# Optimization experiments

Hardware: AMD Instinct MI355X
Metric: run time of the kernel (lower is better)

## Reference

```python
import jax, jax.numpy as jnp
import numpy as np

D_MODEL = 1024
NUM_HEADS = 16
HEAD_DIM = D_MODEL // NUM_HEADS


def setup_inputs() -> dict:
    key = jax.random.key(0)
    k1, k2, k3, k4, k5 = jax.random.split(key, 5)
    scale = 1.0 / np.sqrt(D_MODEL)
    x = jax.random.normal(k1, (2, 2048, D_MODEL), dtype=jnp.float32)
    Wqkv = jax.random.uniform(k2, (D_MODEL, 3 * D_MODEL), jnp.float32, -scale, scale)
    bqkv = jax.random.uniform(k3, (3 * D_MODEL,), jnp.float32, -scale, scale)
    Wout = jax.random.uniform(k4, (D_MODEL, D_MODEL), jnp.float32, -scale, scale)
    bout = jax.random.uniform(k5, (D_MODEL,), jnp.float32, -scale, scale)
    return {"x": x, "Wqkv": Wqkv, "bqkv": bqkv, "Wout": Wout, "bout": bout}


def reference(x, Wqkv, bqkv, Wout, bout):
    B, S, _ = x.shape
    qkv = x @ Wqkv + bqkv                                   # [B, S, 3*D]
    # reshape to [B, S, H, 3*head_dim] then to [B, H, S, 3*head_dim]
    qkv = qkv.reshape(B, S, NUM_HEADS, 3 * HEAD_DIM).transpose(0, 2, 1, 3)
    q, k, v = jnp.split(qkv, 3, axis=-1)                    # each [B, H, S, hd]
    scaled = jnp.einsum("bhqd,bhkd->bhqk", q, k) / jnp.sqrt(jnp.float32(HEAD_DIM))
    attn = jax.nn.softmax(scaled, axis=-1)                  # [B, H, S, S]
    values = jnp.einsum("bhqk,bhkd->bhqd", attn, v)         # [B, H, S, hd]
    values = values.transpose(0, 2, 1, 3).reshape(B, S, D_MODEL)
    return values @ Wout + bout
```

## Files before the change

### kernel.cpp

```cpp
#include <hip/hip_runtime.h>


typedef __attribute__((ext_vector_type(8)))  short short8;
typedef __attribute__((ext_vector_type(4)))  short short4v;
typedef __attribute__((ext_vector_type(8)))  float float8;
typedef __attribute__((ext_vector_type(4)))  float f32x4;
typedef __attribute__((ext_vector_type(16))) float f32x16;
typedef __attribute__((ext_vector_type(4)))  int   int4v;

#define D_MODEL 1024
#define NHEAD   16
#define HD      64
#define SEQ     2048
#define N3      (3*D_MODEL)
#define MB      (1024*1024)

static __device__ __forceinline__ float bf2f(short s) {
    unsigned u = ((unsigned)(unsigned short)s) << 16;
    return __builtin_bit_cast(float, u);
}
static __device__ __forceinline__ short f2bf(float f) {
    unsigned u = __builtin_bit_cast(unsigned, f);
    u = (u + 0x7fff + ((u >> 16) & 1)) >> 16;
    return (short)u;
}
static __device__ __forceinline__ unsigned cvtpk(float a, float b) {
    unsigned r;
    asm("v_cvt_pk_bf16_f32 %0, %1, %2" : "=v"(r) : "v"(a), "v"(b));
    return r;
}
static __device__ __forceinline__ void gl16(const short* g, short* l) {
    __builtin_amdgcn_global_load_lds(
        (const __attribute__((address_space(1))) unsigned int*)g,
        (__attribute__((address_space(3))) unsigned int*)l, 16, 0, 0);
}

__global__ __launch_bounds__(256) void prep(
    const float* __restrict__ x, const float* __restrict__ Wqkv,
    const float* __restrict__ Wout,
    short* __restrict__ Xh, short* __restrict__ Xl,
    short* __restrict__ Wh, short* __restrict__ Wl,
    short* __restrict__ Woh, short* __restrict__ Wol)
{
    __shared__ float tile[32][33];
    const int bid = blockIdx.x;
    const int tid = threadIdx.x;

    if (bid < 2048) {
        const int i = (bid * 256 + tid) * 8;
        const float8 v = *(const float8*)&x[i];
        short8 h, l;
#pragma unroll
        for (int j = 0; j < 8; ++j) {
            h[j] = f2bf(v[j]);
            l[j] = f2bf(v[j] - bf2f(h[j]));
        }
        *(short8*)&Xh[i] = h;
        *(short8*)&Xl[i] = l;
        return;
    }

    const float* in; short *hi, *lo; int K, N, bx, by;
    if (bid < 5120) {
        const int b2 = bid - 2048;
        in = Wqkv; hi = Wh; lo = Wl; K = D_MODEL; N = N3;
        bx = b2 % 96; by = b2 / 96;
    } else {
        const int b3 = bid - 5120;
        in = Wout; hi = Woh; lo = Wol; K = D_MODEL; N = D_MODEL;
        bx = b3 & 31; by = b3 >> 5;
    }
    const int n0 = bx * 32, k0 = by * 32;
    const int tx = tid & 31, ty = tid >> 5;
#pragma unroll
    for (int i = 0; i < 4; ++i)
        tile[ty + 8*i][tx] = in[(k0 + ty + 8*i) * N + (n0 + tx)];
    __syncthreads();
#pragma unroll
    for (int i = 0; i < 4; ++i) {
        const float v  = tile[tx][ty + 8*i];
        const short vh = f2bf(v);
        const short vl = f2bf(v - bf2f(vh));
        const int idx  = (n0 + ty + 8*i) * K + (k0 + tx);
        hi[idx] = vh;
        lo[idx] = vl;
    }
}

#define QBUF_SH 20480
#define OFF_AL  4096
#define OFF_BH  8192
#define OFF_BL  14336

__global__ __launch_bounds__(512, 4) void qkv_gemm8(
    const short* __restrict__ Xh, const short* __restrict__ Xl,
    const short* __restrict__ Bh, const short* __restrict__ Bl,
    const float* __restrict__ bias,
    short* __restrict__ Qo, short* __restrict__ Ko, short* __restrict__ Vt)
{
    __shared__ __attribute__((aligned(16))) short smem[2 * QBUF_SH];

    const int tid  = threadIdx.x;
    const int wave = tid >> 6, lane = tid & 63;
    const int q4 = lane >> 4, l16 = lane & 15;
    const int wr = wave >> 2, wc = wave & 3;
    const int csw = (q4 ^ ((l16 ^ (l16 >> 2)) & 3)) * 8;

    const int flat = blockIdx.x;
    const int sw = (flat & 7) * 64 + (flat >> 3);
    const int mt = sw & 31, nt = sw >> 5;
    const int m0 = mt * 128, n0 = nt * 192;

    const short* srcp[5];
#pragma unroll
    for (int j = 0; j < 5; ++j) {
        const int id = j * 512 + tid;
        int r; const short* mat; int row0;
        if (id < 512)       { r = id >> 2;          mat = Xh; row0 = m0; }
        else if (id < 1024) { r = (id - 512) >> 2;  mat = Xl; row0 = m0; }
        else if (id < 1792) { r = (id - 1024) >> 2; mat = Bh; row0 = n0; }
        else                { r = (id - 1792) >> 2; mat = Bl; row0 = n0; }
        const int cg = (id & 3) ^ ((r ^ (r >> 2)) & 3);
        srcp[j] = &mat[(size_t)(row0 + r) * D_MODEL + cg * 8];
    }

    auto stage = [&](int b) {
#pragma unroll
        for (int j = 0; j < 5; ++j) {
            gl16(srcp[j], smem + b * QBUF_SH + (j * 512 + tid) * 8);
            srcp[j] += 32;
        }
    };

    f32x4 acc[4][3];
#pragma unroll
    for (int i = 0; i < 4; ++i)
#pragma unroll
        for (int j = 0; j < 3; ++j) acc[i][j] = (f32x4){0.f, 0.f, 0.f, 0.f};

    stage(0);
    asm volatile("s_waitcnt vmcnt(0)" ::: "memory");
    __builtin_amdgcn_s_barrier();

    for (int t = 0; t < 32; ++t) {
        const int cur = t & 1;
        const short* base = smem + cur * QBUF_SH;
        const short* Ah_s = base;
        const short* Al_s = base + OFF_AL;
        const short* Bh_s = base + OFF_BH;
        const short* Bl_s = base + OFF_BL;

        short8 bhf[3], blf[3], a0h[2], a0l[2];
#pragma unroll
        for (int n = 0; n < 3; ++n) {
            const int rb = (wc * 48 + n * 16 + l16) * 32 + csw;
            bhf[n] = *(const short8*)(Bh_s + rb);
            blf[n] = *(const short8*)(Bl_s + rb);
        }
#pragma unroll
        for (int ti = 0; ti < 2; ++ti) {
            const int ra = (wr * 64 + ti * 16 + l16) * 32 + csw;
            a0h[ti] = *(const short8*)(Ah_s + ra);
            a0l[ti] = *(const short8*)(Al_s + ra);
        }
        if (t < 31) stage(cur ^ 1);
        __builtin_amdgcn_s_barrier();
        asm volatile("s_waitcnt lgkmcnt(0)" ::: "memory");
        __builtin_amdgcn_sched_barrier(0);
        short8 a1h[2], a1l[2];
#pragma unroll
        for (int ti = 0; ti < 2; ++ti) {
            const int ra = (wr * 64 + (2 + ti) * 16 + l16) * 32 + csw;
            a1h[ti] = *(const short8*)(Ah_s + ra);
            a1l[ti] = *(const short8*)(Al_s + ra);
        }
        __builtin_amdgcn_sched_barrier(0);
        __builtin_amdgcn_s_setprio(1);
#pragma unroll
        for (int ti = 0; ti < 2; ++ti)
#pragma unroll
            for (int n = 0; n < 3; ++n) {
                acc[ti][n] = __builtin_amdgcn_mfma_f32_16x16x32_bf16(a0h[ti], bhf[n], acc[ti][n], 0, 0, 0);
                acc[ti][n] = __builtin_amdgcn_mfma_f32_16x16x32_bf16(a0h[ti], blf[n], acc[ti][n], 0, 0, 0);
                acc[ti][n] = __builtin_amdgcn_mfma_f32_16x16x32_bf16(a0l[ti], bhf[n], acc[ti][n], 0, 0, 0);
            }
        __builtin_amdgcn_s_setprio(0);
        __builtin_amdgcn_s_barrier();

        asm volatile("s_waitcnt lgkmcnt(0)" ::: "memory");
        __builtin_amdgcn_sched_barrier(0);
        __builtin_amdgcn_s_setprio(1);
#pragma unroll
        for (int ti = 0; ti < 2; ++ti)
#pragma unroll
            for (int n = 0; n < 3; ++n) {
                acc[2+ti][n] = __builtin_amdgcn_mfma_f32_16x16x32_bf16(a1h[ti], bhf[n], acc[2+ti][n], 0, 0, 0);
                acc[2+ti][n] = __builtin_amdgcn_mfma_f32_16x16x32_bf16(a1h[ti], blf[n], acc[2+ti][n], 0, 0, 0);
                acc[2+ti][n] = __builtin_amdgcn_mfma_f32_16x16x32_bf16(a1l[ti], bhf[n], acc[2+ti][n], 0, 0, 0);
            }
        __builtin_amdgcn_s_setprio(0);
        asm volatile("s_waitcnt vmcnt(0)" ::: "memory");
        __builtin_amdgcn_s_barrier();
    }

    const float SCALE_Q = 0.125f * 1.4426950408889634f;
#pragma unroll
    for (int tj = 0; tj < 3; ++tj) {
        const int jj = wc * 48 + tj * 16 + l16;
        const int n  = nt * 192 + jj;
        const float bv = bias[n];
#pragma unroll
        for (int ti = 0; ti < 4; ++ti) {
            const int mb = m0 + wr * 64 + ti * 16 + q4 * 4;
            const int b = mb >> 11;
            const int s = mb & 2047;
            const int bh_ = b * NHEAD + nt;
            if (jj >= 128) {
                short4v v4;
#pragma unroll
                for (int r = 0; r < 4; ++r) v4[r] = f2bf(acc[ti][tj][r] + bv);
                *(short4v*)&Vt[(bh_ * HD + (jj - 128)) * SEQ + s] = v4;
            } else if (jj < 64) {
#pragma unroll
                for (int r = 0; r < 4; ++r)
                    Qo[(bh_ * SEQ + s + r) * HD + jj] = f2bf((acc[ti][tj][r] + bv) * SCALE_Q);
            } else {
#pragma unroll
                for (int r = 0; r < 4; ++r)
                    Ko[(bh_ * SEQ + s + r) * HD + (jj - 64)] = f2bf(acc[ti][tj][r] + bv);
            }
        }
    }
}

__global__ __launch_bounds__(256, 2) void attn_tscore(
    const short* __restrict__ Q, const short* __restrict__ K,
    const short* __restrict__ Vt,
    short* __restrict__ Ch, short* __restrict__ Cl)
{
    __shared__ __attribute__((aligned(16))) char smem[36864];
    short (*Ks)[72] = (short(*)[72])smem;
    short (*Vs)[72] = (short(*)[72])(smem + 18432);

    const int bh = blockIdx.x;
    const int qb = blockIdx.y;
    const int bi = bh >> 4, hi_ = bh & 15;

    const short* Qp  = Q  + bh * SEQ * HD;
    const short* Kp  = K  + bh * SEQ * HD;
    const short* Vtp = Vt + bh * HD * SEQ;

    const int tid  = threadIdx.x;
    const int wave = tid >> 6, lane = tid & 63;
    const int l5 = lane & 31, hf = lane >> 5;
    const int q0w = qb * 128 + wave * 32;

    short8 qf[4];
#pragma unroll
    for (int c = 0; c < 4; ++c)
        qf[c] = *(const short8*)&Qp[(q0w + l5) * HD + c * 16 + hf * 8];

    f32x16 oacc0 = (f32x16)(0.f), oacc1 = (f32x16)(0.f);
    float m = -1.0e30f, l = 0.f;

    const int sr = tid >> 2;
    const int sc = (tid & 3) * 16;

    short8 kr0 = *(const short8*)&Kp[sr * HD + sc];
    short8 kr1 = *(const short8*)&Kp[sr * HD + sc + 8];
    short8 vr0 = *(const short8*)&Vtp[sr * SEQ + sc];
    short8 vr1 = *(const short8*)&Vtp[sr * SEQ + sc + 8];
    *(short8*)&Ks[sr][sc]     = kr0;
    *(short8*)&Ks[sr][sc + 8] = kr1;
    *(short8*)&Vs[sr][sc]     = vr0;
    *(short8*)&Vs[sr][sc + 8] = vr1;
    __syncthreads();

    for (int kc = 0; kc < 32; ++kc) {
        const int buf = (kc & 1) << 6;

        if (kc < 31) {
            const int nkb = (kc + 1) << 6;
            kr0 = *(const short8*)&Kp[(nkb + sr) * HD + sc];
            kr1 = *(const short8*)&Kp[(nkb + sr) * HD + sc + 8];
            vr0 = *(const short8*)&Vtp[sr * SEQ + nkb + sc];
            vr1 = *(const short8*)&Vtp[sr * SEQ + nkb + sc + 8];
        }

        f32x16 s0 = (f32x16)(0.f), s1 = (f32x16)(0.f);
#pragma unroll
        for (int c = 0; c < 4; ++c) {
            const short8 ka0 = *(const short8*)&Ks[buf + l5][c * 16 + hf * 8];
            const short8 ka1 = *(const short8*)&Ks[buf + 32 + l5][c * 16 + hf * 8];
            s0 = __builtin_amdgcn_mfma_f32_32x32x16_bf16(ka0, qf[c], s0, 0, 0, 0);
            s1 = __builtin_amdgcn_mfma_f32_32x32x16_bf16(ka1, qf[c], s1, 0, 0, 0);
        }

        float t[8];
#pragma unroll
        for (int i = 0; i < 8; ++i)
            t[i] = fmaxf(fmaxf(s0[i], s0[i + 8]), fmaxf(s1[i], s1[i + 8]));
        float pmax = fmaxf(fmaxf(fmaxf(t[0], t[1]), fmaxf(t[2], t[3])),
                           fmaxf(fmaxf(t[4], t[5]), fmaxf(t[6], t[7])));
        pmax = fmaxf(pmax, __shfl_xor(pmax, 32, 64));

        if (!__all(pmax - m <= 8.0f)) {
            const float mnew  = fmaxf(m, pmax);
            const float alpha = exp2f(m - mnew);
#pragma unroll
            for (int i = 0; i < 16; ++i) { oacc0[i] *= alpha; oacc1[i] *= alpha; }
            l *= alpha;
            m = mnew;
        }

        float p0[16], p1[16];
#pragma unroll
        for (int i = 0; i < 16; ++i) { p0[i] = exp2f(s0[i] - m); p1[i] = exp2f(s1[i] - m); }
        float sa = 0.f, sb = 0.f, sc_ = 0.f, sd = 0.f;
#pragma unroll
        for (int i = 0; i < 4; ++i) {
            sa += p0[i] + p0[i + 8];
            sb += p0[i + 4] + p0[i + 12];
            sc_ += p1[i] + p1[i + 8];
            sd += p1[i + 4] + p1[i + 12];
        }
        float rs = (sa + sb) + (sc_ + sd);
        rs += __shfl_xor(rs, 32, 64);
        l += rs;

        unsigned u0 = cvtpk(p0[0],  p0[1]),  u1 = cvtpk(p0[2],  p0[3]);
        unsigned u2 = cvtpk(p0[4],  p0[5]),  u3 = cvtpk(p0[6],  p0[7]);
        unsigned u4 = cvtpk(p0[8],  p0[9]),  u5 = cvtpk(p0[10], p0[11]);
        unsigned u6 = cvtpk(p0[12], p0[13]), u7 = cvtpk(p0[14], p0[15]);
        unsigned w0 = cvtpk(p1[0],  p1[1]),  w1 = cvtpk(p1[2],  p1[3]);
        unsigned w2 = cvtpk(p1[4],  p1[5]),  w3 = cvtpk(p1[6],  p1[7]);
        unsigned w4 = cvtpk(p1[8],  p1[9]),  w5 = cvtpk(p1[10], p1[11]);
        unsigned w6 = cvtpk(p1[12], p1[13]), w7 = cvtpk(p1[14], p1[15]);
        const unsigned x0 = __shfl_xor(u0, 32, 64), x1 = __shfl_xor(u1, 32, 64);
        const unsigned x2 = __shfl_xor(u2, 32, 64), x3 = __shfl_xor(u3, 32, 64);
        const unsigned x4 = __shfl_xor(u4, 32, 64), x5 = __shfl_xor(u5, 32, 64);
        const unsigned x6 = __shfl_xor(u6, 32, 64), x7 = __shfl_xor(u7, 32, 64);
        const unsigned y0 = __shfl_xor(w0, 32, 64), y1 = __shfl_xor(w1, 32, 64);
        const unsigned y2 = __shfl_xor(w2, 32, 64), y3 = __shfl_xor(w3, 32, 64);
        const unsigned y4 = __shfl_xor(w4, 32, 64), y5 = __shfl_xor(w5, 32, 64);
        const unsigned y6 = __shfl_xor(w6, 32, 64), y7 = __shfl_xor(w7, 32, 64);
        int4v pb0 = (int4v){ (int)(hf ? x2 : u0), (int)(hf ? x3 : u1),
                             (int)(hf ? u2 : x0), (int)(hf ? u3 : x1) };
        int4v pb1 = (int4v){ (int)(hf ? x6 : u4), (int)(hf ? x7 : u5),
                             (int)(hf ? u6 : x4), (int)(hf ? u7 : x5) };
        int4v pb2 = (int4v){ (int)(hf ? y2 : w0), (int)(hf ? y3 : w1),
                             (int)(hf ? w2 : y0), (int)(hf ? w3 : y1) };
        int4v pb3 = (int4v){ (int)(hf ? y6 : w4), (int)(hf ? y7 : w5),
                             (int)(hf ? w6 : y4), (int)(hf ? w7 : y5) };
        const short8 pbf0 = __builtin_bit_cast(short8, pb0);
        const short8 pbf1 = __builtin_bit_cast(short8, pb1);
        const short8 pbf2 = __builtin_bit_cast(short8, pb2);
        const short8 pbf3 = __builtin_bit_cast(short8, pb3);

        {
            const short8 va0 = *(const short8*)&Vs[buf + l5][hf * 8];
            const short8 va1 = *(const short8*)&Vs[buf + l5][16 + hf * 8];
            const short8 va2 = *(const short8*)&Vs[buf + l5][32 + hf * 8];
            const short8 va3 = *(const short8*)&Vs[buf + l5][48 + hf * 8];
            oacc0 = __builtin_amdgcn_mfma_f32_32x32x16_bf16(va0, pbf0, oacc0, 0, 0, 0);
            oacc0 = __builtin_amdgcn_mfma_f32_32x32x16_bf16(va1, pbf1, oacc0, 0, 0, 0);
            oacc0 = __builtin_amdgcn_mfma_f32_32x32x16_bf16(va2, pbf2, oacc0, 0, 0, 0);
            oacc0 = __builtin_amdgcn_mfma_f32_32x32x16_bf16(va3, pbf3, oacc0, 0, 0, 0);
            const short8 vb0 = *(const short8*)&Vs[buf + 32 + l5][hf * 8];
            const short8 vb1 = *(const short8*)&Vs[buf + 32 + l5][16 + hf * 8];
            const short8 vb2 = *(const short8*)&Vs[buf + 32 + l5][32 + hf * 8];
            const short8 vb3 = *(const short8*)&Vs[buf + 32 + l5][48 + hf * 8];
            oacc1 = __builtin_amdgcn_mfma_f32_32x32x16_bf16(vb0, pbf0, oacc1, 0, 0, 0);
            oacc1 = __builtin_amdgcn_mfma_f32_32x32x16_bf16(vb1, pbf1, oacc1, 0, 0, 0);
            oacc1 = __builtin_amdgcn_mfma_f32_32x32x16_bf16(vb2, pbf2, oacc1, 0, 0, 0);
            oacc1 = __builtin_amdgcn_mfma_f32_32x32x16_bf16(vb3, pbf3, oacc1, 0, 0, 0);
        }

        if (kc < 31) {
            const int wb = ((kc + 1) & 1) << 6;
            *(short8*)&Ks[wb + sr][sc]     = kr0;
            *(short8*)&Ks[wb + sr][sc + 8] = kr1;
            *(short8*)&Vs[wb + sr][sc]     = vr0;
            *(short8*)&Vs[wb + sr][sc + 8] = vr1;
        }
        __syncthreads();
    }

    const float inv = 1.0f / l;
#pragma unroll
    for (int i = 0; i < 16; ++i) { oacc0[i] *= inv; oacc1[i] *= inv; }

    float (*epi)[68] = (float(*)[68])(smem + wave * 8704);
#pragma unroll
    for (int r = 0; r < 16; ++r) {
        const int d = (r & 3) + 8 * (r >> 2) + 4 * hf;
        epi[l5][d]      = oacc0[r];
        epi[l5][32 + d] = oacc1[r];
    }
    __builtin_amdgcn_s_waitcnt(0);
#pragma unroll
    for (int pass = 0; pass < 8; ++pass) {
        const int row = pass * 4 + (lane >> 4);
        const int col = (lane & 15) * 4;
        const float4 v = *(const float4*)&epi[row][col];
        const float o[4] = {v.x, v.y, v.z, v.w};
        short4v hh, ll;
#pragma unroll
        for (int i = 0; i < 4; ++i) {
            hh[i] = f2bf(o[i]);
            ll[i] = f2bf(o[i] - bf2f(hh[i]));
        }
        const size_t co = ((size_t)(bi * SEQ + q0w + row)) * D_MODEL + hi_ * HD + col;
        *(short4v*)&Ch[co] = hh;
        *(short4v*)&Cl[co] = ll;
    }
}

__global__ __launch_bounds__(256) void out_gemm128(
    const short* __restrict__ Ah, const short* __restrict__ Al,
    const short* __restrict__ Bh, const short* __restrict__ Bl,
    const float* __restrict__ bias, float* __restrict__ out)
{
    __shared__ short AhS[128*32], AlS[128*32], BhS[128*32], BlS[128*32];

    const int tid  = threadIdx.x;
    const int wave = tid >> 6, lane = tid & 63;
    const int q4 = lane >> 4, l16 = lane & 15;
    const int m0 = blockIdx.y * 128, n0 = blockIdx.x * 128;
    const int rw = (wave & 1) * 64, cw = (wave >> 1) * 64;
    const int trow = tid >> 2;
    const int tcol = (((tid & 3) ^ ((trow ^ (trow >> 2)) & 3))) * 8;
    const int csw = (q4 ^ ((l16 ^ (l16 >> 2)) & 3)) * 8;

    f32x4 acc[4][4];
#pragma unroll
    for (int i = 0; i < 4; ++i)
#pragma unroll
        for (int j = 0; j < 4; ++j) acc[i][j] = (f32x4){0.f, 0.f, 0.f, 0.f};

    for (int kt = 0; kt < D_MODEL; kt += 32) {
        gl16(&Ah[(m0 + trow) * D_MODEL + kt + tcol],      AhS + tid * 8);
        gl16(&Ah[(m0 + 64 + trow) * D_MODEL + kt + tcol], AhS + 2048 + tid * 8);
        gl16(&Al[(m0 + trow) * D_MODEL + kt + tcol],      AlS + tid * 8);
        gl16(&Al[(m0 + 64 + trow) * D_MODEL + kt + tcol], AlS + 2048 + tid * 8);
        gl16(&Bh[(n0 + trow) * D_MODEL + kt + tcol],      BhS + tid * 8);
        gl16(&Bh[(n0 + 64 + trow) * D_MODEL + kt + tcol], BhS + 2048 + tid * 8);
        gl16(&Bl[(n0 + trow) * D_MODEL + kt + tcol],      BlS + tid * 8);
        gl16(&Bl[(n0 + 64 + trow) * D_MODEL + kt + tcol], BlS + 2048 + tid * 8);
        __syncthreads();

        short8 ah[4], al[4], bh[4], bl[4];
#pragma unroll
        for (int t = 0; t < 4; ++t) {
            const int ra = (rw + t * 16 + l16) * 32 + csw;
            const int rb = (cw + t * 16 + l16) * 32 + csw;
            ah[t] = *(const short8*)&AhS[ra];
            al[t] = *(const short8*)&AlS[ra];
            bh[t] = *(const short8*)&BhS[rb];
            bl[t] = *(const short8*)&BlS[rb];
        }
#pragma unroll
        for (int ti = 0; ti < 4; ++ti)
#pragma unroll
            for (int tj = 0; tj < 4; ++tj) {
                acc[ti][tj] = __builtin_amdgcn_mfma_f32_16x16x32_bf16(ah[ti], bh[tj], acc[ti][tj], 0, 0, 0);
                acc[ti][tj] = __builtin_amdgcn_mfma_f32_16x16x32_bf16(ah[ti], bl[tj], acc[ti][tj], 0, 0, 0);
                acc[ti][tj] = __builtin_amdgcn_mfma_f32_16x16x32_bf16(al[ti], bh[tj], acc[ti][tj], 0, 0, 0);
            }
        __syncthreads();
    }

#pragma unroll
    for (int tj = 0; tj < 4; ++tj) {
        const int n = n0 + cw + tj * 16 + l16;
        const float bv = bias[n];
#pragma unroll
        for (int ti = 0; ti < 4; ++ti) {
            const int mb = m0 + rw + ti * 16 + q4 * 4;
#pragma unroll
            for (int r = 0; r < 4; ++r)
                out[(mb + r) * D_MODEL + n] = acc[ti][tj][r] + bv;
        }
    }
}

extern "C" void kernel_launch(void* const* d_in, const int* in_sizes, int n_in,
                              void* d_out, int out_size, void* d_ws, size_t ws_size,
                              hipStream_t stream)
{
    const float* x    = (const float*)d_in[0];
    const float* Wqkv = (const float*)d_in[1];
    const float* bqkv = (const float*)d_in[2];
    const float* Wout = (const float*)d_in[3];
    const float* bout = (const float*)d_in[4];
    float* out = (float*)d_out;

    char* ws = (char*)d_ws;
    short* Qb  = (short*)(ws);
    short* Kb  = (short*)(ws +  8*MB);
    short* Vtb = (short*)(ws + 16*MB);
    short* Woh = (short*)(ws + 24*MB);
    short* Wol = (short*)(ws + 26*MB);
    short* Ch  = (short*)(ws + 28*MB);
    short* Cl  = (short*)(ws + 36*MB);
    short* Xh  = (short*)(ws + 44*MB);
    short* Xl  = (short*)(ws + 52*MB);
    short* Wh  = (short*)(ws + 60*MB);
    short* Wl  = (short*)(ws + 66*MB);

    prep<<<6144, 256, 0, stream>>>(x, Wqkv, Wout, Xh, Xl, Wh, Wl, Woh, Wol);
    qkv_gemm8<<<dim3(512), 512, 0, stream>>>(Xh, Xl, Wh, Wl, bqkv, Qb, Kb, Vtb);
    attn_tscore<<<dim3(32, 16), 256, 0, stream>>>(Qb, Kb, Vtb, Ch, Cl);
    out_gemm128<<<dim3(8, 32), 256, 0, stream>>>(Ch, Cl, Woh, Wol, bout, out);
}
```

Measured before the change: 285.6 us.

## Split attention over two KV halves with merge kernel; use permlane32 swap

The attention kernel now splits the key/value sequence into two halves along a new grid dimension. That doubles the block count from 512 to 1024, to fill the GPU better. Each half writes unnormalized fp32 partial outputs plus running max and sum. A new merge kernel then rescales, combines and emits the bf16 hi/lo split. The 16 cross-half shuffles plus selects are replaced with v_permlane32_swap instructions. The cost is an extra kernel launch, fp32 partial traffic, and workspace aliasing whose buffer reuse ordering must hold.

```diff
diff --git a/kernel.cpp b/kernel.cpp
--- a/kernel.cpp
+++ b/kernel.cpp
@@ -29,6 +29,8 @@
     asm("v_cvt_pk_bf16_f32 %0, %1, %2" : "=v"(r) : "v"(a), "v"(b));
     return r;
 }
+#define PLSWAP(a, b) asm("v_permlane32_swap_b32 %0, %1" : "+v"(a), "+v"(b))
+
 static __device__ __forceinline__ void gl16(const short* g, short* l) {
     __builtin_amdgcn_global_load_lds(
         (const __attribute__((address_space(1))) unsigned int*)g,
@@ -236,19 +238,19 @@
 __global__ __launch_bounds__(256, 2) void attn_tscore(
     const short* __restrict__ Q, const short* __restrict__ K,
     const short* __restrict__ Vt,
-    short* __restrict__ Ch, short* __restrict__ Cl)
+    float* __restrict__ Opart, float2* __restrict__ Ml)
 {
     __shared__ __attribute__((aligned(16))) char smem[36864];
     short (*Ks)[72] = (short(*)[72])smem;
     short (*Vs)[72] = (short(*)[72])(smem + 18432);
 
-    const int bh = blockIdx.x;
-    const int qb = blockIdx.y;
-    const int bi = bh >> 4, hi_ = bh & 15;
-
-    const short* Qp  = Q  + bh * SEQ * HD;
-    const short* Kp  = K  + bh * SEQ * HD;
-    const short* Vtp = Vt + bh * HD * SEQ;
+    const int bh  = blockIdx.x;
+    const int qb  = blockIdx.y;
+    const int kvz = blockIdx.z;
+
+    const short* Qp  = Q  + (size_t)bh * SEQ * HD;
+    const short* Kp  = K  + (size_t)bh * SEQ * HD + (size_t)kvz * 1024 * HD;
+    const short* Vtp = Vt + (size_t)bh * HD * SEQ + (size_t)kvz * 1024;
 
     const int tid  = threadIdx.x;
     const int wave = tid >> 6, lane = tid & 63;
@@ -276,10 +278,10 @@
     *(short8*)&Vs[sr][sc + 8] = vr1;
     __syncthreads();
 
-    for (int kc = 0; kc < 32; ++kc) {
+    for (int kc = 0; kc < 16; ++kc) {
         const int buf = (kc & 1) << 6;
 
-        if (kc < 31) {
+        if (kc < 15) {
             const int nkb = (kc + 1) << 6;
             kr0 = *(const short8*)&Kp[(nkb + sr) * HD + sc];
             kr1 = *(const short8*)&Kp[(nkb + sr) * HD + sc + 8];
@@ -336,22 +338,12 @@
         unsigned w2 = cvtpk(p1[4],  p1[5]),  w3 = cvtpk(p1[6],  p1[7]);
         unsigned w4 = cvtpk(p1[8],  p1[9]),  w5 = cvtpk(p1[10], p1[11]);
         unsigned w6 = cvtpk(p1[12], p1[13]), w7 = cvtpk(p1[14], p1[15]);
-        const unsigned x0 = __shfl_xor(u0, 32, 64), x1 = __shfl_xor(u1, 32, 64);
-        const unsigned x2 = __shfl_xor(u2, 32, 64), x3 = __shfl_xor(u3, 32, 64);
-        const unsigned x4 = __shfl_xor(u4, 32, 64), x5 = __shfl_xor(u5, 32, 64);
-        const unsigned x6 = __shfl_xor(u6, 32, 64), x7 = __shfl_xor(u7, 32, 64);
-        const unsigned y0 = __shfl_xor(w0, 32, 64), y1 = __shfl_xor(w1, 32, 64);
-        const unsigned y2 = __shfl_xor(w2, 32, 64), y3 = __shfl_xor(w3, 32, 64);
-        const unsigned y4 = __shfl_xor(w4, 32, 64), y5 = __shfl_xor(w5, 32, 64);
-        const unsigned y6 = __shfl_xor(w6, 32, 64), y7 = __shfl_xor(w7, 32, 64);
-        int4v pb0 = (int4v){ (int)(hf ? x2 : u0), (int)(hf ? x3 : u1),
-                             (int)(hf ? u2 : x0), (int)(hf ? u3 : x1) };
-        int4v pb1 = (int4v){ (int)(hf ? x6 : u4), (int)(hf ? x7 : u5),
-                             (int)(hf ? u6 : x4), (int)(hf ? u7 : x5) };
-        int4v pb2 = (int4v){ (int)(hf ? y2 : w0), (int)(hf ? y3 : w1),
-                             (int)(hf ? w2 : y0), (int)(hf ? w3 : y1) };
-        int4v pb3 = (int4v){ (int)(hf ? y6 : w4), (int)(hf ? y7 : w5),
-                             (int)(hf ? w6 : y4), (int)(hf ? w7 : y5) };
+        PLSWAP(u0, u2); PLSWAP(u1, u3); PLSWAP(u4, u6); PLSWAP(u5, u7);
+        PLSWAP(w0, w2); PLSWAP(w1, w3); PLSWAP(w4, w6); PLSWAP(w5, w7);
+        int4v pb0 = (int4v){ (int)u0, (int)u1, (int)u2, (int)u3 };
+        int4v pb1 = (int4v){ (int)u4, (int)u5, (int)u6, (int)u7 };
+        int4v pb2 = (int4v){ (int)w0, (int)w1, (int)w2, (int)w3 };
+        int4v pb3 = (int4v){ (int)w4, (int)w5, (int)w6, (int)w7 };
         const short8 pbf0 = __builtin_bit_cast(short8, pb0);
         const short8 pbf1 = __builtin_bit_cast(short8, pb1);
         const short8 pbf2 = __builtin_bit_cast(short8, pb2);
@@ -376,7 +368,7 @@
             oacc1 = __builtin_amdgcn_mfma_f32_32x32x16_bf16(vb3, pbf3, oacc1, 0, 0, 0);
         }
 
-        if (kc < 31) {
+        if (kc < 15) {
             const int wb = ((kc + 1) & 1) << 6;
             *(short8*)&Ks[wb + sr][sc]     = kr0;
             *(short8*)&Ks[wb + sr][sc + 8] = kr1;
@@ -386,29 +378,76 @@
         __syncthreads();
     }
 
-    const float inv = 1.0f / l;
-#pragma unroll
-    for (int i = 0; i < 16; ++i) { oacc0[i] *= inv; oacc1[i] *= inv; }
-
-    float (*epi)[68] = (float(*)[68])(smem + wave * 8704);
+    float* Op = Opart + ((((size_t)kvz * 32 + bh) * 16 + qb) * 4 + wave) * 2048;
+#pragma unroll
+    for (int r = 0; r < 4; ++r) {
+        float4 v;
+        v.x = oacc0[4*r]; v.y = oacc0[4*r+1]; v.z = oacc0[4*r+2]; v.w = oacc0[4*r+3];
+        *(float4*)&Op[r * 256 + lane * 4] = v;
+    }
+#pragma unroll
+    for (int r = 0; r < 4; ++r) {
+        float4 v;
+        v.x = oacc1[4*r]; v.y = oacc1[4*r+1]; v.z = oacc1[4*r+2]; v.w = oacc1[4*r+3];
+        *(float4*)&Op[(4 + r) * 256 + lane * 4] = v;
+    }
+    if (hf == 0) {
+        float2 mv; mv.x = m; mv.y = l;
+        Ml[((size_t)kvz * 32 + bh) * 2048 + q0w + l5] = mv;
+    }
+}
+
+__global__ __launch_bounds__(256) void attn_merge(
+    const float* __restrict__ Opart, const float2* __restrict__ Ml,
+    short* __restrict__ Ch, short* __restrict__ Cl)
+{
+    __shared__ float epi[4][32][68];
+    const int tid = threadIdx.x, wave = tid >> 6, lane = tid & 63;
+    const int l5 = lane & 31, hf = lane >> 5;
+    const int task = blockIdx.x * 4 + wave;
+    const int bh = task >> 6;
+    const int qb = (task >> 2) & 15;
+    const int wq = task & 3;
+    const int bi = bh >> 4, hi_ = bh & 15;
+    const int q0w = qb * 128 + wq * 32;
+
+    const float2 v0 = Ml[(size_t)bh * 2048 + q0w + l5];
+    const float2 v1 = Ml[((size_t)32 + bh) * 2048 + q0w + l5];
+    const float M  = fmaxf(v0.x, v1.x);
+    const float w0 = exp2f(v0.x - M), w1 = exp2f(v1.x - M);
+    const float inv = 1.0f / (v0.y * w0 + v1.y * w1);
+    const float f0 = w0 * inv, f1 = w1 * inv;
+
+    const float* Op0 = Opart + (((size_t)bh * 16 + qb) * 4 + wq) * 2048;
+    const float* Op1 = Opart + ((((size_t)32 + bh) * 16 + qb) * 4 + wq) * 2048;
+    float o[32];
+#pragma unroll
+    for (int r = 0; r < 8; ++r) {
+        const float4 a = *(const float4*)&Op0[r * 256 + lane * 4];
+        const float4 b = *(const float4*)&Op1[r * 256 + lane * 4];
+        o[4*r]   = a.x * f0 + b.x * f1;
+        o[4*r+1] = a.y * f0 + b.y * f1;
+        o[4*r+2] = a.z * f0 + b.z * f1;
+        o[4*r+3] = a.w * f0 + b.w * f1;
+    }
 #pragma unroll
     for (int r = 0; r < 16; ++r) {
         const int d = (r & 3) + 8 * (r >> 2) + 4 * hf;
-        epi[l5][d]      = oacc0[r];
-        epi[l5][32 + d] = oacc1[r];
+        epi[wave][l5][d]      = o[r];
+        epi[wave][l5][32 + d] = o[16 + r];
     }
     __builtin_amdgcn_s_waitcnt(0);
 #pragma unroll
     for (int pass = 0; pass < 8; ++pass) {
         const int row = pass * 4 + (lane >> 4);
         const int col = (lane & 15) * 4;
-        const float4 v = *(const float4*)&epi[row][col];
-        const float o[4] = {v.x, v.y, v.z, v.w};
+        const float4 v = *(const float4*)&epi[wave][row][col];
+        const float ov[4] = {v.x, v.y, v.z, v.w};
         short4v hh, ll;
 #pragma unroll
         for (int i = 0; i < 4; ++i) {
-            hh[i] = f2bf(o[i]);
-            ll[i] = f2bf(o[i] - bf2f(hh[i]));
+            hh[i] = f2bf(ov[i]);
+            ll[i] = f2bf(ov[i] - bf2f(hh[i]));
         }
         const size_t co = ((size_t)(bi * SEQ + q0w + row)) * D_MODEL + hi_ * HD + col;
         *(short4v*)&Ch[co] = hh;
@@ -496,20 +535,23 @@
     float* out = (float*)d_out;
 
     char* ws = (char*)d_ws;
-    short* Qb  = (short*)(ws);
-    short* Kb  = (short*)(ws +  8*MB);
-    short* Vtb = (short*)(ws + 16*MB);
-    short* Woh = (short*)(ws + 24*MB);
-    short* Wol = (short*)(ws + 26*MB);
-    short* Ch  = (short*)(ws + 28*MB);
-    short* Cl  = (short*)(ws + 36*MB);
-    short* Xh  = (short*)(ws + 44*MB);
-    short* Xl  = (short*)(ws + 52*MB);
-    short* Wh  = (short*)(ws + 60*MB);
-    short* Wl  = (short*)(ws + 66*MB);
+    short*  Woh   = (short*)(ws);
+    short*  Wol   = (short*)(ws +  2*MB);
+    short*  Qb    = (short*)(ws +  4*MB);
+    short*  Kb    = (short*)(ws + 12*MB);
+    short*  Vtb   = (short*)(ws + 20*MB);
+    float*  Opart = (float*)(ws + 28*MB);
+    float2* Ml    = (float2*)(ws + 60*MB);
+    short*  Ch    = (short*)(ws +  4*MB);
+    short*  Cl    = (short*)(ws + 12*MB);
+    short*  Xh    = (short*)(ws + 28*MB);
+    short*  Xl    = (short*)(ws + 36*MB);
+    short*  Wh    = (short*)(ws + 44*MB);
+    short*  Wl    = (short*)(ws + 50*MB);
 
     prep<<<6144, 256, 0, stream>>>(x, Wqkv, Wout, Xh, Xl, Wh, Wl, Woh, Wol);
     qkv_gemm8<<<dim3(512), 512, 0, stream>>>(Xh, Xl, Wh, Wl, bqkv, Qb, Kb, Vtb);
-    attn_tscore<<<dim3(32, 16), 256, 0, stream>>>(Qb, Kb, Vtb, Ch, Cl);
+    attn_tscore<<<dim3(32, 16, 2), 256, 0, stream>>>(Qb, Kb, Vtb, Opart, Ml);
+    attn_merge<<<512, 256, 0, stream>>>(Opart, Ml, Ch, Cl);
     out_gemm128<<<dim3(8, 32), 256, 0, stream>>>(Ch, Cl, Woh, Wol, bout, out);
 }
```

Measured after the change: 275.8 us. -3.4%, faster.
